# Kernel tuning notes

Measured on AMD Instinct MI355X. Metric: run time of the kernel, lower is better.

The kernel has to match this reference:

```python
import jax, jax.numpy as jnp
import numpy as np

DIM = 768
H = 12  # num_heads -> head width W = 64 (required by internal reshapes)


def setup_inputs() -> dict:
    key = jax.random.key(0)
    ks = jax.random.split(key, 16)
    B, S = 1, 128  # V = Q = A = 128 tokens
    d = {
        "v": jax.random.normal(ks[0], (B, S, DIM), jnp.float32),
        "q": jax.random.normal(ks[1], (B, S, DIM), jnp.float32),
        "a": jax.random.normal(ks[2], (B, S, DIM), jnp.float32),
        "v_mask": jnp.ones((B, S), jnp.bool_),  # unused by the module, kept for signature parity
        "q_mask": jnp.ones((B, S), jnp.bool_),
        "a_mask": jnp.ones((B, S), jnp.bool_),
    }
    scale = 0.02
    names = ["Wv", "Wq", "Wa", "Wvo", "Wqo", "Wao"]
    for i, n in enumerate(names):
        d[n] = jax.random.normal(ks[3 + i], (DIM, DIM), jnp.float32) * scale
        d["b" + n[1:].lower()] = jnp.zeros((DIM,), jnp.float32)
    return d


def _heads(x):
    # (B, S, D) -> (B, H, S, W)
    B, S, D = x.shape
    return x.reshape(B, S, H, D // H).transpose(0, 2, 1, 3)


def reference(v, q, a, v_mask, q_mask, a_mask,
              Wv, bv, Wq, bq, Wa, ba, Wvo, bvo, Wqo, bqo, Wao, bao):
    B, Sv, D = v.shape
    Sq, Sa = q.shape[1], a.shape[1]
    W = D // H
    nv, nq, na = Sv // 8, Sq // 8, Sa // 8

    # first projections (masks are unused in the original forward)
    vp = v @ Wv + bv
    qp = q @ Wq + bq
    ap = a @ Wa + ba
    # output projections are applied to the ALREADY-projected tensors (as in source)
    vo = vp @ Wvo + bvo
    qo = qp @ Wqo + bqo
    ao = ap @ Wao + bao

    vh, qh, ah = _heads(vp), _heads(qp), _heads(ap)          # (B,H,S,W)
    voh, qoh, aoh = _heads(vo), _heads(qo), _heads(ao)

    # trilinear scores: (B,H,V,Q,A)
    att = jnp.einsum('bhvw,bhqw,bhaw->bhvqa', vh, qh, ah) / jnp.sqrt(jnp.asarray(W, vh.dtype))
    K = nv * nq * na
    # faithful to source: view(-1, H, nv*nq*na) then softmax over last axis, view back
    att = jax.nn.softmax(att.reshape(-1, H, K), axis=-1)
    att = att.reshape(-1, H, nv, nq, na)  # dropout p=0 -> identity
    B2 = att.shape[0]

    # source uses att.size(2) (= nv) for ALL three reshapes (requires V=Q=A)
    vor = voh.reshape(B2, H, nv, -1)
    qor = qoh.reshape(B2, H, nv, -1)
    aor = aoh.reshape(B2, H, nv, -1)

    v_out = jnp.einsum('bhvqa,bhvw->bvhw', att, vor).reshape(-1, DIM)
    q_out = jnp.einsum('bhvqa,bhqw->bqhw', att, qor).reshape(-1, DIM)
    a_out = jnp.einsum('bhvqa,bhaw->bahw', att, aor).reshape(-1, DIM)
    return (v_out, q_out, a_out)
```

## Files before the change

kernel.cpp:

```cpp
#include <hip/hip_runtime.h>


#define DIM   768
#define SEQ   128
#define NH    12
#define HW    64
#define PROJ_ELEMS (SEQ * DIM)
#define WELEMS     (DIM * DIM)
#define QOUT_OFF   98304
#define AOUT_OFF   196608

typedef _Float16 f16x8 __attribute__((ext_vector_type(8)));
typedef float    f32x4 __attribute__((ext_vector_type(4)));

__global__ __launch_bounds__(256) void prep_kernel(
    const float* __restrict__ v, const float* __restrict__ q, const float* __restrict__ a,
    const float* __restrict__ W0, const float* __restrict__ W1, const float* __restrict__ W2,
    const float* __restrict__ W3, const float* __restrict__ W4, const float* __restrict__ W5,
    _Float16* __restrict__ Wt,
    _Float16* __restrict__ vI, _Float16* __restrict__ qI, _Float16* __restrict__ aI)
{
    const int z = blockIdx.z;
    const int t = threadIdx.x;
    if (z < 6) {
        const float* W = (z == 0) ? W0 : (z == 1) ? W1 : (z == 2) ? W2
                       : (z == 3) ? W3 : (z == 4) ? W4 : W5;
        _Float16* WtM = Wt + z * WELEMS;
        __shared__ _Float16 T[64][72];
        const int k0 = blockIdx.x * 64;
        const int n0 = blockIdx.y * 64;
        const int c4 = (t & 15) * 4;
        #pragma unroll
        for (int p = 0; p < 4; ++p) {
            const int r = (t >> 4) + 16 * p;
            f32x4 wv = *(const f32x4*)&W[(k0 + r) * DIM + n0 + c4];
            T[c4 + 0][r] = (_Float16)wv[0];
            T[c4 + 1][r] = (_Float16)wv[1];
            T[c4 + 2][r] = (_Float16)wv[2];
            T[c4 + 3][r] = (_Float16)wv[3];
        }
        __syncthreads();
        const int c2 = (t & 7) * 8;
        #pragma unroll
        for (int p = 0; p < 2; ++p) {
            const int r = (t >> 3) + 32 * p;
            *(f16x8*)&WtM[(n0 + r) * DIM + k0 + c2] = *(const f16x8*)&T[r][c2];
        }
    } else {
        const int bid = blockIdx.x + 12 * blockIdx.y;
        const int mat = bid / 48;
        const int off = (bid - mat * 48) * 2048 + t * 8;
        const float* src = (mat == 0) ? v : (mat == 1) ? q : a;
        _Float16* dst    = (mat == 0) ? vI : (mat == 1) ? qI : aI;
        f32x4 lo = *(const f32x4*)&src[off];
        f32x4 hi = *(const f32x4*)&src[off + 4];
        f16x8 o;
        o[0] = (_Float16)lo[0]; o[1] = (_Float16)lo[1];
        o[2] = (_Float16)lo[2]; o[3] = (_Float16)lo[3];
        o[4] = (_Float16)hi[0]; o[5] = (_Float16)hi[1];
        o[6] = (_Float16)hi[2]; o[7] = (_Float16)hi[3];
        *(f16x8*)&dst[off] = o;
    }
}

__global__ __launch_bounds__(256) void proj_kernel(
    const _Float16* __restrict__ A0, const _Float16* __restrict__ A1, const _Float16* __restrict__ A2,
    const _Float16* __restrict__ T0, const _Float16* __restrict__ T1, const _Float16* __restrict__ T2,
    const float* __restrict__ b0, const float* __restrict__ b1, const float* __restrict__ b2,
    void* __restrict__ C0, void* __restrict__ C1, void* __restrict__ C2,
    int out_f16)
{
    const int mat = blockIdx.y;
    const _Float16* __restrict__ A = (mat == 0) ? A0 : (mat == 1) ? A1 : A2;
    const _Float16* __restrict__ T = (mat == 0) ? T0 : (mat == 1) ? T1 : T2;
    const float* __restrict__ bb   = (mat == 0) ? b0 : (mat == 1) ? b1 : b2;
    void* __restrict__ C           = (mat == 0) ? C0 : (mat == 1) ? C1 : C2;

    const int n0   = blockIdx.x * 32;
    const int t    = threadIdx.x;
    const int w    = t >> 6;
    const int lane = t & 63;
    const int fm   = lane & 15;
    const int fk   = (lane >> 4) << 3;

    const _Float16* pa0 = A + (32 * w + fm) * DIM + fk;
    const _Float16* pa1 = pa0 + 16 * DIM;
    const _Float16* pb0 = T + (n0 + fm) * DIM + fk;
    const _Float16* pb1 = pb0 + 16 * DIM;

    f32x4 acc[2][2];
    #pragma unroll
    for (int i = 0; i < 2; ++i)
        #pragma unroll
        for (int j = 0; j < 2; ++j) acc[i][j] = (f32x4){0.f, 0.f, 0.f, 0.f};

    #pragma unroll 4
    for (int s = 0; s < 24; ++s) {
        const f16x8 a0 = *(const f16x8*)(pa0 + 32 * s);
        const f16x8 a1 = *(const f16x8*)(pa1 + 32 * s);
        const f16x8 w0 = *(const f16x8*)(pb0 + 32 * s);
        const f16x8 w1 = *(const f16x8*)(pb1 + 32 * s);
        acc[0][0] = __builtin_amdgcn_mfma_f32_16x16x32_f16(a0, w0, acc[0][0], 0, 0, 0);
        acc[0][1] = __builtin_amdgcn_mfma_f32_16x16x32_f16(a0, w1, acc[0][1], 0, 0, 0);
        acc[1][0] = __builtin_amdgcn_mfma_f32_16x16x32_f16(a1, w0, acc[1][0], 0, 0, 0);
        acc[1][1] = __builtin_amdgcn_mfma_f32_16x16x32_f16(a1, w1, acc[1][1], 0, 0, 0);
    }

    const int quad4 = (lane >> 4) << 2;
    #pragma unroll
    for (int mt = 0; mt < 2; ++mt) {
        const int row0 = 32 * w + 16 * mt + quad4;
        #pragma unroll
        for (int nt = 0; nt < 2; ++nt) {
            const int col = n0 + 16 * nt + fm;
            const float bi = bb[col];
            #pragma unroll
            for (int rr = 0; rr < 4; ++rr) {
                const float val = acc[mt][nt][rr] + bi;
                if (out_f16) ((_Float16*)C)[(row0 + rr) * DIM + col] = (_Float16)val;
                else         ((float*)C)[(row0 + rr) * DIM + col]    = val;
            }
        }
    }
}

__device__ __forceinline__ float fetch_o(const float* __restrict__ p, int idx) {
    return p[((idx >> 6) & 127) * DIM + (idx >> 13) * HW + (idx & 63)];
}

__global__ __launch_bounds__(256) void fused_attn_kernel(
    const _Float16* __restrict__ vpH, const _Float16* __restrict__ qpH,
    const _Float16* __restrict__ apH,
    const float* __restrict__ vo, const float* __restrict__ qo, const float* __restrict__ ao,
    float* __restrict__ out)
{
    const int vtok = blockIdx.x;
    const int h    = blockIdx.y;

    __shared__ _Float16 vqL[128][72];

    const int t    = threadIdx.x;
    const int w    = t >> 6;
    const int lane = t & 63;
    const int fm   = lane & 15;
    const int fk   = (lane >> 4) << 3;

    {
        const int r  = t >> 1;
        const int kh = (t & 1) << 5;
        const _Float16* pq = qpH + r    * DIM + h * HW + kh;
        const _Float16* pv = vpH + vtok * DIM + h * HW + kh;
        #pragma unroll
        for (int u = 0; u < 4; ++u) {
            const f16x8 qv = *(const f16x8*)(pq + 8 * u);
            const f16x8 vv = *(const f16x8*)(pv + 8 * u);
            *(f16x8*)&vqL[r][kh + 8 * u] = qv * vv;
        }
    }
    __syncthreads();

    f32x4 acc[2][8];
    #pragma unroll
    for (int qt = 0; qt < 2; ++qt)
        #pragma unroll
        for (int at = 0; at < 8; ++at)
            acc[qt][at] = (f32x4){0.f, 0.f, 0.f, 0.f};

    const int q0 = 32 * w;
    #pragma unroll
    for (int ks = 0; ks < 2; ++ks) {
        const f16x8 af0 = *(const f16x8*)&vqL[q0 + fm     ][32 * ks + fk];
        const f16x8 af1 = *(const f16x8*)&vqL[q0 + 16 + fm][32 * ks + fk];
        #pragma unroll
        for (int at = 0; at < 8; ++at) {
            const f16x8 bf = *(const f16x8*)&apH[(16 * at + fm) * DIM + h * HW + 32 * ks + fk];
            acc[0][at] = __builtin_amdgcn_mfma_f32_16x16x32_f16(af0, bf, acc[0][at], 0, 0, 0);
            acc[1][at] = __builtin_amdgcn_mfma_f32_16x16x32_f16(af1, bf, acc[1][at], 0, 0, 0);
        }
    }

    float sv[2][2] = {{0.f, 0.f}, {0.f, 0.f}};
    float sq[2][8];
    #pragma unroll
    for (int i = 0; i < 2; ++i)
        #pragma unroll
        for (int j = 0; j < 8; ++j) sq[i][j] = 0.f;
    float sa = 0.f;
    #pragma unroll
    for (int qt = 0; qt < 2; ++qt)
        #pragma unroll
        for (int at = 0; at < 8; ++at)
            #pragma unroll
            for (int rr = 0; rr < 4; ++rr) {
                const float e = __expf(acc[qt][at][rr] * 0.125f);
                sv[qt][rr >> 1] += e;
                sq[rr & 1][at]  += e;
                sa += e;
            }

    sa += __shfl_xor(sa, 16);
    sa += __shfl_xor(sa, 32);
    float tot = sa;
    tot += __shfl_xor(tot, 1);
    tot += __shfl_xor(tot, 2);
    tot += __shfl_xor(tot, 4);
    tot += __shfl_xor(tot, 8);
    const bool b0 = lane & 1;
    const bool b1 = lane & 2;
    float sF;
    {
        float snd0 = b0 ? sv[0][0] : sv[1][0];
        float snd1 = b0 ? sv[0][1] : sv[1][1];
        float r0 = __shfl_xor(snd0, 1);
        float r1 = __shfl_xor(snd1, 1);
        float s0 = (b0 ? sv[1][0] : sv[0][0]) + r0;
        float s1 = (b0 ? sv[1][1] : sv[0][1]) + r1;
        float snd = b1 ? s0 : s1;
        float r2 = __shfl_xor(snd, 2);
        sF = (b1 ? s1 : s0) + r2;
    }
    sF += __shfl_xor(sF, 4);
    sF += __shfl_xor(sF, 8);
    float s[16];
    #pragma unroll
    for (int i = 0; i < 2; ++i)
        #pragma unroll
        for (int j = 0; j < 8; ++j) s[i * 8 + j] = sq[i][j];
    #pragma unroll
    for (int k = 0; k < 4; ++k) {
        const int d = 1 << k;
        const int m = 16 >> (k + 1);
        const bool b = (lane >> k) & 1;
        #pragma unroll
        for (int x = 0; x < m; ++x) {
            const float snd = b ? s[x] : s[x + m];
            const float rcv = __shfl_xor(snd, d);
            s[x] = (b ? s[x + m] : s[x]) + rcv;
        }
    }
    s[0] += __shfl_xor(s[0], 16);
    s[0] += __shfl_xor(s[0], 32);

    const int g  = h * 512 + vtok * 4 + w;
    const int b2 = g / 12;
    const int h2 = g - b2 * 12;
    const float invZ = 1.0f / tot;

    if (fm < 4) {
        const int quad = lane >> 4;
        const int bin  = (fm & 1) * 8 + quad * 2 + ((fm >> 1) & 1);
        out[(b2 * 16 + bin) * 12 + h2] = sF * invZ * fetch_o(vo, g * 16 + bin);
    }
    if (lane < 16) {
        const int qbin = 8 * (lane & 1) + 4 * ((lane >> 1) & 1)
                       + 2 * ((lane >> 2) & 1) + (lane >> 3);
        out[QOUT_OFF + (b2 * 16 + qbin) * 12 + h2] =
            s[0] * invZ * fetch_o(qo, g * 16 + qbin);
        out[AOUT_OFF + (b2 * 16 + lane) * 12 + h2] =
            sa * invZ * fetch_o(ao, g * 16 + lane);
    }
}

extern "C" void kernel_launch(void* const* d_in, const int* in_sizes, int n_in,
                              void* d_out, int out_size, void* d_ws, size_t ws_size,
                              hipStream_t stream)
{
    const float* v   = (const float*)d_in[0];
    const float* q   = (const float*)d_in[1];
    const float* a   = (const float*)d_in[2];
    const float* Wv  = (const float*)d_in[6];
    const float* bv  = (const float*)d_in[7];
    const float* Wq  = (const float*)d_in[8];
    const float* bq  = (const float*)d_in[9];
    const float* Wa  = (const float*)d_in[10];
    const float* ba  = (const float*)d_in[11];
    const float* Wvo = (const float*)d_in[12];
    const float* bvo = (const float*)d_in[13];
    const float* Wqo = (const float*)d_in[14];
    const float* bqo = (const float*)d_in[15];
    const float* Wao = (const float*)d_in[16];
    const float* bao = (const float*)d_in[17];

    float* out = (float*)d_out;

    _Float16* Wt  = (_Float16*)d_ws;
    _Float16* vI  = Wt + 6 * WELEMS;
    _Float16* qI  = vI + PROJ_ELEMS;
    _Float16* aI  = qI + PROJ_ELEMS;
    _Float16* vpH = aI + PROJ_ELEMS;
    _Float16* qpH = vpH + PROJ_ELEMS;
    _Float16* apH = qpH + PROJ_ELEMS;
    float*    vo  = (float*)(apH + PROJ_ELEMS);
    float*    qo  = vo + PROJ_ELEMS;
    float*    ao  = qo + PROJ_ELEMS;

    prep_kernel<<<dim3(12, 12, 7), 256, 0, stream>>>(
        v, q, a, Wv, Wq, Wa, Wvo, Wqo, Wao, Wt, vI, qI, aI);
    proj_kernel<<<dim3(24, 3), 256, 0, stream>>>(
        vI, qI, aI, Wt, Wt + WELEMS, Wt + 2 * WELEMS,
        bv, bq, ba, vpH, qpH, apH, 1);
    proj_kernel<<<dim3(24, 3), 256, 0, stream>>>(
        vpH, qpH, apH, Wt + 3 * WELEMS, Wt + 4 * WELEMS, Wt + 5 * WELEMS,
        bvo, bqo, bao, vo, qo, ao, 0);
    fused_attn_kernel<<<dim3(SEQ, NH), 256, 0, stream>>>(
        vpH, qpH, apH, vo, qo, ao, out);
}
```

Baseline: 158.7 us.

## Split projection GEMM into single-wave 16x16 tiles and stage A-head in LDS

The projection kernel changes from 72 four-wave blocks with 32x32-per-wave tiles to 1152 single-wave blocks, each computing one 16x16 output tile. This fills more compute units on this small GEMM but gives up operand reuse, so each A and W row is refetched more often. The attention kernel now stages the per-head A projection in shared memory once per block instead of re-reading it from global memory in the MFMA loop. The output gather index is also simplified to a direct base-plus-offset form.

```diff
diff --git a/kernel.cpp b/kernel.cpp
--- a/kernel.cpp
+++ b/kernel.cpp
@@ -63,98 +63,78 @@
     }
 }
 
-__global__ __launch_bounds__(256) void proj_kernel(
+__global__ __launch_bounds__(64) void proj_kernel(
     const _Float16* __restrict__ A0, const _Float16* __restrict__ A1, const _Float16* __restrict__ A2,
     const _Float16* __restrict__ T0, const _Float16* __restrict__ T1, const _Float16* __restrict__ T2,
     const float* __restrict__ b0, const float* __restrict__ b1, const float* __restrict__ b2,
     void* __restrict__ C0, void* __restrict__ C1, void* __restrict__ C2,
     int out_f16)
 {
-    const int mat = blockIdx.y;
+    const int mat = blockIdx.z;
     const _Float16* __restrict__ A = (mat == 0) ? A0 : (mat == 1) ? A1 : A2;
     const _Float16* __restrict__ T = (mat == 0) ? T0 : (mat == 1) ? T1 : T2;
     const float* __restrict__ bb   = (mat == 0) ? b0 : (mat == 1) ? b1 : b2;
     void* __restrict__ C           = (mat == 0) ? C0 : (mat == 1) ? C1 : C2;
 
-    const int n0   = blockIdx.x * 32;
+    const int m0   = blockIdx.x * 16;
+    const int n0   = blockIdx.y * 16;
+    const int lane = threadIdx.x & 63;
+    const int fm   = lane & 15;
+    const int fk   = (lane >> 4) << 3;
+
+    const _Float16* pa = A + (m0 + fm) * DIM + fk;
+    const _Float16* pb = T + (n0 + fm) * DIM + fk;
+
+    f32x4 acc = (f32x4){0.f, 0.f, 0.f, 0.f};
+    #pragma unroll
+    for (int s = 0; s < 24; ++s) {
+        const f16x8 af = *(const f16x8*)(pa + 32 * s);
+        const f16x8 wf = *(const f16x8*)(pb + 32 * s);
+        acc = __builtin_amdgcn_mfma_f32_16x16x32_f16(af, wf, acc, 0, 0, 0);
+    }
+
+    const int col  = n0 + fm;
+    const int row0 = m0 + ((lane >> 4) << 2);
+    const float bi = bb[col];
+    #pragma unroll
+    for (int rr = 0; rr < 4; ++rr) {
+        const float val = acc[rr] + bi;
+        if (out_f16) ((_Float16*)C)[(row0 + rr) * DIM + col] = (_Float16)val;
+        else         ((float*)C)[(row0 + rr) * DIM + col]    = val;
+    }
+}
+
+__global__ __launch_bounds__(256) void fused_attn_kernel(
+    const _Float16* __restrict__ vpH, const _Float16* __restrict__ qpH,
+    const _Float16* __restrict__ apH,
+    const float* __restrict__ vo, const float* __restrict__ qo, const float* __restrict__ ao,
+    float* __restrict__ out)
+{
+    const int vtok = blockIdx.x;
+    const int h    = blockIdx.y;
+
+    __shared__ _Float16 vqL[128][72];
+    __shared__ _Float16 ahL[128][72];
+
     const int t    = threadIdx.x;
     const int w    = t >> 6;
     const int lane = t & 63;
     const int fm   = lane & 15;
     const int fk   = (lane >> 4) << 3;
 
-    const _Float16* pa0 = A + (32 * w + fm) * DIM + fk;
-    const _Float16* pa1 = pa0 + 16 * DIM;
-    const _Float16* pb0 = T + (n0 + fm) * DIM + fk;
-    const _Float16* pb1 = pb0 + 16 * DIM;
-
-    f32x4 acc[2][2];
-    #pragma unroll
-    for (int i = 0; i < 2; ++i)
-        #pragma unroll
-        for (int j = 0; j < 2; ++j) acc[i][j] = (f32x4){0.f, 0.f, 0.f, 0.f};
-
-    #pragma unroll 4
-    for (int s = 0; s < 24; ++s) {
-        const f16x8 a0 = *(const f16x8*)(pa0 + 32 * s);
-        const f16x8 a1 = *(const f16x8*)(pa1 + 32 * s);
-        const f16x8 w0 = *(const f16x8*)(pb0 + 32 * s);
-        const f16x8 w1 = *(const f16x8*)(pb1 + 32 * s);
-        acc[0][0] = __builtin_amdgcn_mfma_f32_16x16x32_f16(a0, w0, acc[0][0], 0, 0, 0);
-        acc[0][1] = __builtin_amdgcn_mfma_f32_16x16x32_f16(a0, w1, acc[0][1], 0, 0, 0);
-        acc[1][0] = __builtin_amdgcn_mfma_f32_16x16x32_f16(a1, w0, acc[1][0], 0, 0, 0);
-        acc[1][1] = __builtin_amdgcn_mfma_f32_16x16x32_f16(a1, w1, acc[1][1], 0, 0, 0);
-    }
-
-    const int quad4 = (lane >> 4) << 2;
-    #pragma unroll
-    for (int mt = 0; mt < 2; ++mt) {
-        const int row0 = 32 * w + 16 * mt + quad4;
-        #pragma unroll
-        for (int nt = 0; nt < 2; ++nt) {
-            const int col = n0 + 16 * nt + fm;
-            const float bi = bb[col];
-            #pragma unroll
-            for (int rr = 0; rr < 4; ++rr) {
-                const float val = acc[mt][nt][rr] + bi;
-                if (out_f16) ((_Float16*)C)[(row0 + rr) * DIM + col] = (_Float16)val;
-                else         ((float*)C)[(row0 + rr) * DIM + col]    = val;
-            }
-        }
-    }
-}
-
-__device__ __forceinline__ float fetch_o(const float* __restrict__ p, int idx) {
-    return p[((idx >> 6) & 127) * DIM + (idx >> 13) * HW + (idx & 63)];
-}
-
-__global__ __launch_bounds__(256) void fused_attn_kernel(
-    const _Float16* __restrict__ vpH, const _Float16* __restrict__ qpH,
-    const _Float16* __restrict__ apH,
-    const float* __restrict__ vo, const float* __restrict__ qo, const float* __restrict__ ao,
-    float* __restrict__ out)
-{
-    const int vtok = blockIdx.x;
-    const int h    = blockIdx.y;
-
-    __shared__ _Float16 vqL[128][72];
-
-    const int t    = threadIdx.x;
-    const int w    = t >> 6;
-    const int lane = t & 63;
-    const int fm   = lane & 15;
-    const int fk   = (lane >> 4) << 3;
-
     {
         const int r  = t >> 1;
         const int kh = (t & 1) << 5;
         const _Float16* pq = qpH + r    * DIM + h * HW + kh;
         const _Float16* pv = vpH + vtok * DIM + h * HW + kh;
+        const _Float16* pa = apH + r    * DIM + h * HW + kh;
         #pragma unroll
         for (int u = 0; u < 4; ++u) {
             const f16x8 qv = *(const f16x8*)(pq + 8 * u);
             const f16x8 vv = *(const f16x8*)(pv + 8 * u);
+            const f16x8 av = *(const f16x8*)(pa + 8 * u);
             *(f16x8*)&vqL[r][kh + 8 * u] = qv * vv;
+            *(f16x8*)&ahL[r][kh + 8 * u] = av;
         }
     }
     __syncthreads();
@@ -173,7 +153,7 @@
         const f16x8 af1 = *(const f16x8*)&vqL[q0 + 16 + fm][32 * ks + fk];
         #pragma unroll
         for (int at = 0; at < 8; ++at) {
-            const f16x8 bf = *(const f16x8*)&apH[(16 * at + fm) * DIM + h * HW + 32 * ks + fk];
+            const f16x8 bf = *(const f16x8*)&ahL[16 * at + fm][32 * ks + fk];
             acc[0][at] = __builtin_amdgcn_mfma_f32_16x16x32_f16(af0, bf, acc[0][at], 0, 0, 0);
             acc[1][at] = __builtin_amdgcn_mfma_f32_16x16x32_f16(af1, bf, acc[1][at], 0, 0, 0);
         }
@@ -245,19 +225,18 @@
     const int b2 = g / 12;
     const int h2 = g - b2 * 12;
     const float invZ = 1.0f / tot;
+    const int obase = vtok * DIM + h * HW + w * 16;
 
     if (fm < 4) {
         const int quad = lane >> 4;
         const int bin  = (fm & 1) * 8 + quad * 2 + ((fm >> 1) & 1);
-        out[(b2 * 16 + bin) * 12 + h2] = sF * invZ * fetch_o(vo, g * 16 + bin);
+        out[(b2 * 16 + bin) * 12 + h2] = sF * invZ * vo[obase + bin];
     }
     if (lane < 16) {
         const int qbin = 8 * (lane & 1) + 4 * ((lane >> 1) & 1)
                        + 2 * ((lane >> 2) & 1) + (lane >> 3);
-        out[QOUT_OFF + (b2 * 16 + qbin) * 12 + h2] =
-            s[0] * invZ * fetch_o(qo, g * 16 + qbin);
-        out[AOUT_OFF + (b2 * 16 + lane) * 12 + h2] =
-            sa * invZ * fetch_o(ao, g * 16 + lane);
+        out[QOUT_OFF + (b2 * 16 + qbin) * 12 + h2] = s[0] * invZ * qo[obase + qbin];
+        out[AOUT_OFF + (b2 * 16 + lane) * 12 + h2] = sa   * invZ * ao[obase + lane];
     }
 }
 
@@ -296,10 +275,10 @@
 
     prep_kernel<<<dim3(12, 12, 7), 256, 0, stream>>>(
         v, q, a, Wv, Wq, Wa, Wvo, Wqo, Wao, Wt, vI, qI, aI);
-    proj_kernel<<<dim3(24, 3), 256, 0, stream>>>(
+    proj_kernel<<<dim3(8, 48, 3), 64, 0, stream>>>(
         vI, qI, aI, Wt, Wt + WELEMS, Wt + 2 * WELEMS,
         bv, bq, ba, vpH, qpH, apH, 1);
-    proj_kernel<<<dim3(24, 3), 256, 0, stream>>>(
+    proj_kernel<<<dim3(8, 48, 3), 64, 0, stream>>>(
         vpH, qpH, apH, Wt + 3 * WELEMS, Wt + 4 * WELEMS, Wt + 5 * WELEMS,
         bvo, bqo, bao, vo, qo, ao, 0);
     fused_attn_kernel<<<dim3(SEQ, NH), 256, 0, stream>>>(
```

Result: faster. 137.1 us (-13.6%).
